# Optimization experiments

Hardware: AMD Instinct MI355X
Metric: run time of the kernel (lower is better)

The kernel has to match this reference:

```python
import jax, jax.numpy as jnp
import numpy as np

N = 50000          # nodes (len(sample.x))
E = 1600000        # edges, avg degree 32
F_IN = 64          # sample.num_node_features
CH = 32            # 4 * 4 * channels_optuna(2)
K = 30000          # ceil(0.6 * N), TopKPooling keep count
FINAL_NODES = 2


def _gelu(v):
    return jax.nn.gelu(v, approximate=False)  # torch F.gelu uses exact erf


def _w(key, shape):
    return jax.random.normal(key, shape, jnp.float32) / np.sqrt(shape[0]).astype(np.float32)


def setup_inputs() -> dict:
    key = jax.random.key(0)
    ks = jax.random.split(key, 16)
    return {
        "x": jax.random.normal(ks[0], (N, F_IN), jnp.float32),
        "edge_index": jax.random.randint(ks[1], (2, E), 0, N, dtype=jnp.int32),
        "wd_root": _w(ks[2], (F_IN, 4)),
        "wd_b": jnp.zeros((4,), jnp.float32),
        "w0_rel": _w(ks[3], (4, CH)),
        "w0_root": _w(ks[4], (4, CH)),
        "w0_b": jnp.zeros((CH,), jnp.float32),
        "w1_rel": _w(ks[5], (CH, 2 * CH)),
        "w1_root": _w(ks[6], (CH, 2 * CH)),
        "w1_b": jnp.zeros((2 * CH,), jnp.float32),
        "w2_rel": _w(ks[7], (2 * CH, 4 * CH)),
        "w2_root": _w(ks[8], (2 * CH, 4 * CH)),
        "w2_b": jnp.zeros((4 * CH,), jnp.float32),
        "pool_p": jax.random.normal(ks[9], (4 * CH,), jnp.float32),
        "w3_rel": _w(ks[10], (4 * CH, 8 * CH)),
        "w3_root": _w(ks[11], (4 * CH, 8 * CH)),
        "w3_b": jnp.zeros((8 * CH,), jnp.float32),
        "w_out": _w(ks[12], (FINAL_NODES * 8 * CH, 1)),
        "b_out": jnp.zeros((1,), jnp.float32),
    }


def _graph_conv(x, src, dst, w_rel, w_root, b, n, mask=None):
    # PyG GraphConv: out_i = W_root x_i + W_rel * sum_{j->i} x_j + b
    msg = x[src]
    if mask is not None:
        msg = msg * mask[:, None]
    agg = jax.ops.segment_sum(msg, dst, num_segments=n)
    return agg @ w_rel + x @ w_root + b


def reference(x, edge_index, wd_root, wd_b, w0_rel, w0_root, w0_b,
              w1_rel, w1_root, w1_b, w2_rel, w2_root, w2_b, pool_p,
              w3_rel, w3_root, w3_b, w_out, b_out):
    src, dst = edge_index[0], edge_index[1]
    # dense_input is GraphConv with empty edge set -> only root term + bias
    h = _gelu(x @ wd_root + wd_b)                                   # [N, 4]
    h = _gelu(_graph_conv(h, src, dst, w0_rel, w0_root, w0_b, N))   # [N, 32]
    h = _gelu(_graph_conv(h, src, dst, w1_rel, w1_root, w1_b, N))   # [N, 64]
    h = _gelu(_graph_conv(h, src, dst, w2_rel, w2_root, w2_b, N))   # [N, 128]
    # TopKPooling(ratio=0.6): score = tanh(x.p/||p||), keep top-K, gate kept x
    score = jnp.tanh(h @ pool_p / jnp.linalg.norm(pool_p))          # [N]
    vals, perm = jax.lax.top_k(score, K)
    hk = h[perm] * vals[:, None]                                    # [K, 128]
    # filter_adj: keep edges with both endpoints selected, remap indices
    node_map = jnp.full((N,), -1, jnp.int32).at[perm].set(jnp.arange(K, dtype=jnp.int32))
    s2, d2 = node_map[src], node_map[dst]
    valid = (s2 >= 0) & (d2 >= 0)
    mask = valid.astype(hk.dtype)
    s2 = jnp.where(valid, s2, 0)
    d2 = jnp.where(valid, d2, 0)
    h2 = _gelu(_graph_conv(hk, s2, d2, w3_rel, w3_root, w3_b, K, mask=mask))  # [K, 256]
    # avg_pool_x with cluster = i % final_nodes (single graph batch)
    cluster = jnp.arange(K, dtype=jnp.int32) % FINAL_NODES
    sums = jax.ops.segment_sum(h2, cluster, num_segments=FINAL_NODES)
    counts = jax.ops.segment_sum(jnp.ones((K,), h2.dtype), cluster, num_segments=FINAL_NODES)
    pooled = sums / counts[:, None]                                  # [2, 256]
    return pooled.reshape(-1) @ w_out + b_out                        # [1]
```

## Files before the change

### kernel.cpp

```cpp
#include <hip/hip_runtime.h>
#include <hip/hip_bf16.h>
#include <math.h>

#define NN 50000
#define EE 1600000
#define KK 30000
#define RTILE 1088
#define NTILES 48
#define CHUNK 16384
#define GBLK 98
#define BKT 391
#define CMAX 6144

typedef __attribute__((ext_vector_type(8))) short bf16x8;
typedef __attribute__((ext_vector_type(4))) float f32x4;

__device__ __forceinline__ float gelu_f(float v) {
  return 0.5f * v * (1.0f + erff(v * 0.70710678118654752440f));
}

__device__ __forceinline__ unsigned short f2bf(float x) {
  __hip_bfloat16 h = __float2bfloat16(x);
  return *(unsigned short*)&h;
}

__device__ __forceinline__ float bf2f(unsigned u16) {
  return __uint_as_float(u16 << 16);
}

__global__ __launch_bounds__(1024) void k_scanA(const unsigned* __restrict__ in, unsigned* __restrict__ out,
                                                unsigned* __restrict__ bsum, int n) {
  __shared__ unsigned sh[1024];
  int t = threadIdx.x;
  int i = blockIdx.x * 1024 + t;
  unsigned v = (i < n) ? in[i] : 0u;
  sh[t] = v;
  __syncthreads();
  for (int ofs = 1; ofs < 1024; ofs <<= 1) {
    unsigned add = (t >= ofs) ? sh[t - ofs] : 0u;
    __syncthreads();
    sh[t] += add;
    __syncthreads();
  }
  if (i < n) out[i] = sh[t] - v;
  if (t == 1023) bsum[blockIdx.x] = sh[1023];
}

__global__ __launch_bounds__(1024) void k_scanB(unsigned* __restrict__ bsum, int nb) {
  __shared__ unsigned sh[1024];
  int t = threadIdx.x;
  unsigned v = (t < nb) ? bsum[t] : 0u;
  sh[t] = v;
  __syncthreads();
  for (int ofs = 1; ofs < 1024; ofs <<= 1) {
    unsigned add = (t >= ofs) ? sh[t - ofs] : 0u;
    __syncthreads();
    sh[t] += add;
    __syncthreads();
  }
  if (t < nb) bsum[t] = sh[t] - v;
}

__global__ __launch_bounds__(1024) void k_scanC(unsigned* __restrict__ out, const unsigned* __restrict__ bsum, int n) {
  int i = blockIdx.x * 1024 + threadIdx.x;
  if (i < n) out[i] += bsum[blockIdx.x];
}

__global__ __launch_bounds__(512) void k_binA(const int* __restrict__ src, const int* __restrict__ dst,
                                              unsigned* __restrict__ chunkEdges, int* __restrict__ chunkBase) {
  __shared__ int hist[BKT];
  __shared__ int scanb[512];
  __shared__ unsigned buf[CHUNK];
  int t = threadIdx.x, g = blockIdx.x;
  int e0 = g * CHUNK;
  int n = EE - e0; if (n > CHUNK) n = CHUNK;
  for (int i = t; i < BKT; i += 512) hist[i] = 0;
  __syncthreads();
  for (int i = t; i < n; i += 512) atomicAdd(&hist[dst[e0 + i] >> 7], 1);
  __syncthreads();
  int v = (t < BKT) ? hist[t] : 0;
  scanb[t] = v;
  __syncthreads();
  for (int ofs = 1; ofs < 512; ofs <<= 1) {
    int a = (t >= ofs) ? scanb[t - ofs] : 0;
    __syncthreads();
    scanb[t] += a;
    __syncthreads();
  }
  if (t < BKT) {
    scanb[t] -= v;
    chunkBase[g * (BKT + 1) + t] = scanb[t];
    hist[t] = 0;
  }
  if (t == 0) chunkBase[g * (BKT + 1) + BKT] = n;
  __syncthreads();
  for (int i = t; i < n; i += 512) {
    int d = dst[e0 + i], s = src[e0 + i];
    int b = d >> 7;
    int pos = scanb[b] + atomicAdd(&hist[b], 1);
    buf[pos] = ((unsigned)(d & 127) << 16) | (unsigned)s;
  }
  __syncthreads();
  for (int i = t; i < n; i += 512) chunkEdges[e0 + i] = buf[i];
}

__global__ __launch_bounds__(512) void k_bktsum(const int* __restrict__ chunkBase, unsigned* __restrict__ bktBase) {
  __shared__ unsigned sh[512];
  int t = threadIdx.x;
  unsigned s = 0;
  if (t < BKT) {
    for (int g = 0; g < GBLK; g++)
      s += (unsigned)(chunkBase[g * (BKT + 1) + t + 1] - chunkBase[g * (BKT + 1) + t]);
  }
  sh[t] = s;
  __syncthreads();
  for (int ofs = 1; ofs < 512; ofs <<= 1) {
    unsigned a = (t >= ofs) ? sh[t - ofs] : 0u;
    __syncthreads();
    sh[t] += a;
    __syncthreads();
  }
  if (t < BKT) bktBase[t] = sh[t] - s;
  if (t == 0) bktBase[BKT] = EE;
}

__global__ __launch_bounds__(256) void k_binC(const unsigned* __restrict__ chunkEdges, const int* __restrict__ chunkBase,
                                              const unsigned* __restrict__ bktBase,
                                              int* __restrict__ rowp, int* __restrict__ csr) {
  __shared__ int segS[GBLK + 1];
  __shared__ int cnt[128];
  __shared__ int loc[128];
  __shared__ unsigned eBuf[CMAX];
  __shared__ int csrB[CMAX];
  int t = threadIdx.x, b = blockIdx.x;
  int n0 = b << 7;
  int nb = NN - n0; if (nb > 128) nb = 128;
  if (t < GBLK) segS[t] = chunkBase[t * (BKT + 1) + b + 1] - chunkBase[t * (BKT + 1) + b];
  if (t < 128) cnt[t] = 0;
  __syncthreads();
  if (t == 0) {
    int run = 0;
    for (int g = 0; g < GBLK; g++) { int L = segS[g]; segS[g] = run; run += L; }
    segS[GBLK] = run;
  }
  __syncthreads();
  int total = segS[GBLK];
  for (int i = t; i < total; i += 256) {
    int lo = 0, hi = GBLK - 1;
    while (lo < hi) { int mid = (lo + hi + 1) >> 1; if (segS[mid] <= i) lo = mid; else hi = mid - 1; }
    int off = chunkBase[lo * (BKT + 1) + b] + (i - segS[lo]);
    unsigned v = chunkEdges[lo * CHUNK + off];
    if (i < CMAX) eBuf[i] = v;
    atomicAdd(&cnt[v >> 16], 1);
  }
  __syncthreads();
  if (t < 128) loc[t] = cnt[t];
  __syncthreads();
  for (int ofs = 1; ofs < 128; ofs <<= 1) {
    int a = (t < 128 && t >= ofs) ? loc[t - ofs] : 0;
    __syncthreads();
    if (t < 128) loc[t] += a;
    __syncthreads();
  }
  if (t < 128) loc[t] -= cnt[t];
  __syncthreads();
  int base = (int)bktBase[b];
  if (t < nb) rowp[n0 + t] = base + loc[t];
  if (b == BKT - 1 && t == 0) rowp[NN] = base + total;
  if (t < 128) cnt[t] = 0;
  __syncthreads();
  for (int i = t; i < total && i < CMAX; i += 256) {
    unsigned v = eBuf[i];
    int d = (int)(v >> 16);
    int pos = loc[d] + atomicAdd(&cnt[d], 1);
    if (pos < CMAX) csrB[pos] = (int)(v & 0xFFFFu);
  }
  __syncthreads();
  for (int i = t; i < total && i < CMAX; i += 256) csr[base + i] = csrB[i];
}

__global__ __launch_bounds__(256) void k_dense(const float* __restrict__ x, const float* __restrict__ w,
                                               const float* __restrict__ b, float* __restrict__ h0) {
  __shared__ float ws[260];
  int t = threadIdx.x;
  ws[t] = w[t];
  if (t < 4) ws[256 + t] = b[t];
  __syncthreads();
  int n = blockIdx.x * 256 + t;
  if (n >= NN) return;
  float acc0 = ws[256], acc1 = ws[257], acc2 = ws[258], acc3 = ws[259];
  const float4* xr = (const float4*)(x + (size_t)n * 64);
#pragma unroll
  for (int k4 = 0; k4 < 16; k4++) {
    float4 v = xr[k4];
    const float* wk = &ws[k4 * 16];
    acc0 += v.x * wk[0];  acc1 += v.x * wk[1];  acc2 += v.x * wk[2];  acc3 += v.x * wk[3];
    acc0 += v.y * wk[4];  acc1 += v.y * wk[5];  acc2 += v.y * wk[6];  acc3 += v.y * wk[7];
    acc0 += v.z * wk[8];  acc1 += v.z * wk[9];  acc2 += v.z * wk[10]; acc3 += v.z * wk[11];
    acc0 += v.w * wk[12]; acc1 += v.w * wk[13]; acc2 += v.w * wk[14]; acc3 += v.w * wk[15];
  }
  float4 o;
  o.x = gelu_f(acc0); o.y = gelu_f(acc1); o.z = gelu_f(acc2); o.w = gelu_f(acc3);
  ((float4*)h0)[n] = o;
}

template <int TPN>
__global__ __launch_bounds__(256) void k_agg(const float* __restrict__ h, const int* __restrict__ rowp,
                                             const int* __restrict__ csr, float* __restrict__ agg) {
  long gt = (long)blockIdx.x * 256 + threadIdx.x;
  int n = (int)(gt / TPN), lane = (int)(gt % TPN);
  if (n >= NN) return;
  int beg = rowp[n], end = rowp[n + 1];
  const float4* hv = (const float4*)h;
  float4 a0 = make_float4(0.f, 0.f, 0.f, 0.f), a1 = a0, a2 = a0, a3 = a0;
  int e = beg;
  for (; e + 4 <= end; e += 4) {
    int s0 = csr[e], s1 = csr[e + 1], s2 = csr[e + 2], s3 = csr[e + 3];
    float4 v0 = hv[(size_t)s0 * TPN + lane];
    float4 v1 = hv[(size_t)s1 * TPN + lane];
    float4 v2 = hv[(size_t)s2 * TPN + lane];
    float4 v3 = hv[(size_t)s3 * TPN + lane];
    a0.x += v0.x; a0.y += v0.y; a0.z += v0.z; a0.w += v0.w;
    a1.x += v1.x; a1.y += v1.y; a1.z += v1.z; a1.w += v1.w;
    a2.x += v2.x; a2.y += v2.y; a2.z += v2.z; a2.w += v2.w;
    a3.x += v3.x; a3.y += v3.y; a3.z += v3.z; a3.w += v3.w;
  }
  for (; e < end; e++) {
    int s = csr[e];
    float4 v = hv[(size_t)s * TPN + lane];
    a0.x += v.x; a0.y += v.y; a0.z += v.z; a0.w += v.w;
  }
  float4 acc;
  acc.x = (a0.x + a1.x) + (a2.x + a3.x);
  acc.y = (a0.y + a1.y) + (a2.y + a3.y);
  acc.z = (a0.z + a1.z) + (a2.z + a3.z);
  acc.w = (a0.w + a1.w) + (a2.w + a3.w);
  ((float4*)agg)[(size_t)n * TPN + lane] = acc;
}

__global__ __launch_bounds__(256) void k_gemm0(const float* __restrict__ agg0, const float* __restrict__ h0,
                                               const float* __restrict__ wrel, const float* __restrict__ wroot,
                                               const float* __restrict__ bias, float* __restrict__ h1) {
  __shared__ float ws[288];
  int t = threadIdx.x;
  if (t < 128) { ws[t] = wrel[t]; ws[128 + t] = wroot[t]; }
  if (t < 32) ws[256 + t] = bias[t];
  __syncthreads();
  int gt = blockIdx.x * 256 + t;
  int n = gt >> 5, j = gt & 31;
  if (n >= NN) return;
  float4 a = ((const float4*)agg0)[n];
  float4 h = ((const float4*)h0)[n];
  float acc = ws[256 + j];
  acc += a.x * ws[j]        + a.y * ws[32 + j]  + a.z * ws[64 + j]  + a.w * ws[96 + j];
  acc += h.x * ws[128 + j]  + h.y * ws[160 + j] + h.z * ws[192 + j] + h.w * ws[224 + j];
  h1[(size_t)n * 32 + j] = gelu_f(acc);
}

template <int DIN, int DOUT>
__global__ __launch_bounds__(256) void k_gemm(const float* __restrict__ Ag, const float* __restrict__ Hp,
                                              const float* __restrict__ Wrel, const float* __restrict__ Wroot,
                                              const float* __restrict__ bias, float* __restrict__ Cout, int R) {
  constexpr int JQ = DOUT / 64;
  __shared__ float As[32][64];
  __shared__ float Ws[32][DOUT];
  int t = threadIdx.x;
  int tx = t & 15, ty = t >> 4;
  int n0 = blockIdx.x * 64;
  int an = t & 63, ac = t >> 6;
  int rowA = n0 + an;
  float acc[JQ][4][4] = {};
  for (int kc = 0; kc < 2 * DIN; kc += 32) {
#pragma unroll
    for (int i = 0; i < 8; i++) {
      int k = ac + 4 * i;
      int kk = kc + k;
      float av = 0.f;
      if (rowA < R) {
        av = (kk < DIN) ? Ag[(size_t)rowA * DIN + kk]
                        : Hp[(size_t)rowA * DIN + (kk - DIN)];
      }
      As[k][an] = av;
    }
    {
      const float* Wsrc = (kc < DIN) ? (Wrel + (size_t)kc * DOUT)
                                     : (Wroot + (size_t)(kc - DIN) * DOUT);
#pragma unroll
      for (int i = 0; i < DOUT / 32; i++) {
        int lin = i * 256 + t;
        int k = lin / (DOUT / 4);
        int col = (lin % (DOUT / 4)) * 4;
        float4 wv = *(const float4*)&Wsrc[(size_t)k * DOUT + col];
        *(float4*)&Ws[k][col] = wv;
      }
    }
    __syncthreads();
#pragma unroll
    for (int k = 0; k < 32; k++) {
      float4 a = *(const float4*)&As[k][4 * ty];
#pragma unroll
      for (int jq = 0; jq < JQ; jq++) {
        float4 w = *(const float4*)&Ws[k][jq * 64 + 4 * tx];
        acc[jq][0][0] += a.x * w.x; acc[jq][0][1] += a.x * w.y; acc[jq][0][2] += a.x * w.z; acc[jq][0][3] += a.x * w.w;
        acc[jq][1][0] += a.y * w.x; acc[jq][1][1] += a.y * w.y; acc[jq][1][2] += a.y * w.z; acc[jq][1][3] += a.y * w.w;
        acc[jq][2][0] += a.z * w.x; acc[jq][2][1] += a.z * w.y; acc[jq][2][2] += a.z * w.z; acc[jq][2][3] += a.z * w.w;
        acc[jq][3][0] += a.w * w.x; acc[jq][3][1] += a.w * w.y; acc[jq][3][2] += a.w * w.z; acc[jq][3][3] += a.w * w.w;
      }
    }
    __syncthreads();
  }
#pragma unroll
  for (int jq = 0; jq < JQ; jq++) {
    int j = jq * 64 + 4 * tx;
#pragma unroll
    for (int r = 0; r < 4; r++) {
      int row = n0 + 4 * ty + r;
      if (row < R) {
        float4 o;
        o.x = gelu_f(acc[jq][r][0] + bias[j]);
        o.y = gelu_f(acc[jq][r][1] + bias[j + 1]);
        o.z = gelu_f(acc[jq][r][2] + bias[j + 2]);
        o.w = gelu_f(acc[jq][r][3] + bias[j + 3]);
        *(float4*)&Cout[(size_t)row * DOUT + j] = o;
      }
    }
  }
}

__global__ __launch_bounds__(256) void k_score(const float* __restrict__ h3, const float* __restrict__ p,
                                               float* __restrict__ score, unsigned* __restrict__ skey,
                                               unsigned* __restrict__ hist) {
  __shared__ float red[256];
  int t = threadIdx.x;
  float pv = 0.f;
  if (t < 128) { float q = p[t]; pv = q * q; }
  red[t] = pv;
  __syncthreads();
  for (int s = 128; s > 0; s >>= 1) { if (t < s) red[t] += red[t + s]; __syncthreads(); }
  float pinv = rsqrtf(red[0]);
  int n = blockIdx.x * 8 + (t >> 5);
  int lane = t & 31;
  if (n >= NN) return;
  float4 hv = ((const float4*)(h3 + (size_t)n * 128))[lane];
  float4 pw = ((const float4*)p)[lane];
  float d = hv.x * pw.x + hv.y * pw.y + hv.z * pw.z + hv.w * pw.w;
  for (int o = 16; o > 0; o >>= 1) d += __shfl_xor(d, o, 32);
  if (lane == 0) {
    float sc = tanhf(d * pinv);
    score[n] = sc;
    unsigned bits = __float_as_uint(sc);
    unsigned mono = (bits & 0x80000000u) ? ~bits : (bits | 0x80000000u);
    unsigned sk = ~mono;
    skey[n] = sk;
    atomicAdd(&hist[(size_t)(n / RTILE) * 65536 + (sk & 0xFFFFu)], 1u);
  }
}

template <int SHIFT>
__global__ __launch_bounds__(256) void k_rhist(const unsigned* __restrict__ keyIn, unsigned* __restrict__ histMat) {
  int gid = blockIdx.x * 256 + threadIdx.x;
  if (gid < NN) {
    unsigned d = (keyIn[gid] >> SHIFT) & 0xFFFFu;
    int tile = gid / RTILE;
    atomicAdd(&histMat[(size_t)tile * 65536 + d], 1u);
  }
}

__global__ __launch_bounds__(256) void k_rtileprefix(unsigned* __restrict__ histMat, unsigned* __restrict__ total) {
  int d = blockIdx.x * 256 + threadIdx.x;
  unsigned run = 0;
  for (int tl = 0; tl < NTILES; tl++) {
    size_t ix = (size_t)tl * 65536 + d;
    unsigned v = histMat[ix];
    histMat[ix] = run;
    run += v;
  }
  total[d] = run;
}

template <int SHIFT, bool FIRST>
__global__ __launch_bounds__(64) void k_rscatter(const unsigned* __restrict__ keyIn, const unsigned* __restrict__ idIn,
                                                 unsigned* __restrict__ histMat, const unsigned* __restrict__ base,
                                                 unsigned* __restrict__ keyOut, unsigned* __restrict__ idOut) {
  int t = threadIdx.x;
  int tile = blockIdx.x;
  for (int c = 0; c < RTILE / 64; c++) {
    int idx = tile * RTILE + c * 64 + t;
    int valid = idx < NN;
    unsigned key = 0u, id = 0u;
    if (valid) {
      key = keyIn[idx];
      id = FIRST ? (unsigned)idx : idIn[idx];
    }
    unsigned d = (key >> SHIFT) & 0xFFFFu;
    unsigned long long same = __ballot(valid != 0);
    if (!valid) same = ~same;
#pragma unroll
    for (int b = 0; b < 16; b++) {
      unsigned long long bb = __ballot((int)((d >> b) & 1u));
      same &= ((d >> b) & 1u) ? bb : ~bb;
    }
    unsigned long long lower = (t == 0) ? 0ull : (same << (64 - t) >> (64 - t));
    unsigned intrar = (unsigned)__popcll(lower);
    unsigned total = (unsigned)__popcll(same);
    int leader = (int)(__ffsll((long long)same) - 1);
    unsigned old = 0u;
    if (valid && t == leader) old = atomicAdd(&histMat[(size_t)tile * 65536 + d], total);
    unsigned basec = (unsigned)__shfl((int)old, leader, 64);
    if (valid) {
      unsigned pos = base[d] + basec + intrar;
      keyOut[pos] = key;
      idOut[pos] = id;
    }
  }
}

__global__ __launch_bounds__(64) void k_rscatter2(const unsigned* __restrict__ keyIn, const unsigned* __restrict__ idIn,
                                                  unsigned* __restrict__ histMat, const unsigned* __restrict__ base,
                                                  int* __restrict__ rank, int* __restrict__ inv) {
  int t = threadIdx.x;
  int tile = blockIdx.x;
  for (int c = 0; c < RTILE / 64; c++) {
    int idx = tile * RTILE + c * 64 + t;
    int valid = idx < NN;
    unsigned key = 0u, id = 0u;
    if (valid) {
      key = keyIn[idx];
      id = idIn[idx];
    }
    unsigned d = key >> 16;
    unsigned long long same = __ballot(valid != 0);
    if (!valid) same = ~same;
#pragma unroll
    for (int b = 0; b < 16; b++) {
      unsigned long long bb = __ballot((int)((d >> b) & 1u));
      same &= ((d >> b) & 1u) ? bb : ~bb;
    }
    unsigned long long lower = (t == 0) ? 0ull : (same << (64 - t) >> (64 - t));
    unsigned intrar = (unsigned)__popcll(lower);
    unsigned total = (unsigned)__popcll(same);
    int leader = (int)(__ffsll((long long)same) - 1);
    unsigned old = 0u;
    if (valid && t == leader) old = atomicAdd(&histMat[(size_t)tile * 65536 + d], total);
    unsigned basec = (unsigned)__shfl((int)old, leader, 64);
    if (valid) {
      unsigned pos = base[d] + basec + intrar;
      rank[(int)id] = (int)pos;
      if (pos < KK) inv[pos] = (int)id;
    }
  }
}

__global__ __launch_bounds__(256) void k_agg3(const int* __restrict__ rank, const int* __restrict__ rowp,
                                              const int* __restrict__ csr, unsigned short* __restrict__ A16) {
  long gt = (long)blockIdx.x * 256 + threadIdx.x;
  int n = (int)(gt >> 4), lane = (int)(gt & 15);
  if (n >= NN) return;
  int r = rank[n];
  if (r >= KK) return;
  int beg = rowp[n], end = rowp[n + 1];
  float a0 = 0.f, a1 = 0.f, a2 = 0.f, a3 = 0.f, a4 = 0.f, a5 = 0.f, a6 = 0.f, a7 = 0.f;
  int e = beg;
  for (; e + 4 <= end; e += 4) {
    int s0 = csr[e], s1 = csr[e + 1], s2 = csr[e + 2], s3 = csr[e + 3];
    int r0 = rank[s0], r1 = rank[s1], r2 = rank[s2], r3 = rank[s3];
    r0 = min(r0, KK); r1 = min(r1, KK); r2 = min(r2, KK); r3 = min(r3, KK);
    uint4 v0 = *(const uint4*)&A16[(size_t)r0 * 256 + 128 + lane * 8];
    uint4 v1 = *(const uint4*)&A16[(size_t)r1 * 256 + 128 + lane * 8];
    uint4 v2 = *(const uint4*)&A16[(size_t)r2 * 256 + 128 + lane * 8];
    uint4 v3 = *(const uint4*)&A16[(size_t)r3 * 256 + 128 + lane * 8];
    a0 += bf2f(v0.x & 0xFFFFu) + bf2f(v1.x & 0xFFFFu) + bf2f(v2.x & 0xFFFFu) + bf2f(v3.x & 0xFFFFu);
    a1 += bf2f(v0.x >> 16)     + bf2f(v1.x >> 16)     + bf2f(v2.x >> 16)     + bf2f(v3.x >> 16);
    a2 += bf2f(v0.y & 0xFFFFu) + bf2f(v1.y & 0xFFFFu) + bf2f(v2.y & 0xFFFFu) + bf2f(v3.y & 0xFFFFu);
    a3 += bf2f(v0.y >> 16)     + bf2f(v1.y >> 16)     + bf2f(v2.y >> 16)     + bf2f(v3.y >> 16);
    a4 += bf2f(v0.z & 0xFFFFu) + bf2f(v1.z & 0xFFFFu) + bf2f(v2.z & 0xFFFFu) + bf2f(v3.z & 0xFFFFu);
    a5 += bf2f(v0.z >> 16)     + bf2f(v1.z >> 16)     + bf2f(v2.z >> 16)     + bf2f(v3.z >> 16);
    a6 += bf2f(v0.w & 0xFFFFu) + bf2f(v1.w & 0xFFFFu) + bf2f(v2.w & 0xFFFFu) + bf2f(v3.w & 0xFFFFu);
    a7 += bf2f(v0.w >> 16)     + bf2f(v1.w >> 16)     + bf2f(v2.w >> 16)     + bf2f(v3.w >> 16);
  }
  for (; e < end; e++) {
    int s = csr[e];
    int rs = min(rank[s], KK);
    uint4 v = *(const uint4*)&A16[(size_t)rs * 256 + 128 + lane * 8];
    a0 += bf2f(v.x & 0xFFFFu); a1 += bf2f(v.x >> 16);
    a2 += bf2f(v.y & 0xFFFFu); a3 += bf2f(v.y >> 16);
    a4 += bf2f(v.z & 0xFFFFu); a5 += bf2f(v.z >> 16);
    a6 += bf2f(v.w & 0xFFFFu); a7 += bf2f(v.w >> 16);
  }
  uint4 o;
  o.x = (unsigned)f2bf(a0) | ((unsigned)f2bf(a1) << 16);
  o.y = (unsigned)f2bf(a2) | ((unsigned)f2bf(a3) << 16);
  o.z = (unsigned)f2bf(a4) | ((unsigned)f2bf(a5) << 16);
  o.w = (unsigned)f2bf(a6) | ((unsigned)f2bf(a7) << 16);
  *(uint4*)&A16[(size_t)r * 256 + lane * 8] = o;
}

__global__ __launch_bounds__(256) void k_gate(const float* __restrict__ h3, const float* __restrict__ scor,
                                              const int* __restrict__ inv, unsigned short* __restrict__ A16) {
  int gt = blockIdx.x * 256 + threadIdx.x;
  int r = gt >> 4, lane = gt & 15;
  if (r > KK) return;
  if (r == KK) {
    *(uint4*)&A16[(size_t)KK * 256 + 128 + lane * 8] = make_uint4(0u, 0u, 0u, 0u);
    return;
  }
  int nd = inv[r];
  float g = scor[nd];
  const float4* src = (const float4*)&h3[(size_t)nd * 128 + lane * 8];
  float4 v0 = src[0], v1 = src[1];
  uint4 o;
  o.x = (unsigned)f2bf(v0.x * g) | ((unsigned)f2bf(v0.y * g) << 16);
  o.y = (unsigned)f2bf(v0.z * g) | ((unsigned)f2bf(v0.w * g) << 16);
  o.z = (unsigned)f2bf(v1.x * g) | ((unsigned)f2bf(v1.y * g) << 16);
  o.w = (unsigned)f2bf(v1.z * g) | ((unsigned)f2bf(v1.w * g) << 16);
  *(uint4*)&A16[(size_t)r * 256 + 128 + lane * 8] = o;
}

__global__ __launch_bounds__(256) void k_wcvt(const float* __restrict__ w3rel, const float* __restrict__ w3root,
                                              unsigned short* __restrict__ W16) {
  int idx = blockIdx.x * 256 + threadIdx.x;
  int k = idx >> 8, c = idx & 255;
  float v = (k < 128) ? w3rel[(size_t)k * 256 + c] : w3root[(size_t)(k - 128) * 256 + c];
  W16[(size_t)c * 256 + k] = f2bf(v);
}

__global__ __launch_bounds__(256) void k_gemm3m(const unsigned short* __restrict__ A16,
                                                const unsigned short* __restrict__ W16,
                                                const float* __restrict__ bias,
                                                float* __restrict__ psum) {
  __shared__ unsigned short Al[64][40];
  __shared__ unsigned short Bl[256][40];
  __shared__ float red[512];
  int t = threadIdx.x;
  int wv = t >> 6, l = t & 63;
  int n0 = blockIdx.x * 64;
  f32x4 acc[4][4];
#pragma unroll
  for (int m = 0; m < 4; m++)
#pragma unroll
    for (int n = 0; n < 4; n++) acc[m][n] = (f32x4){0.f, 0.f, 0.f, 0.f};
  for (int k0 = 0; k0 < 256; k0 += 32) {
    {
      int row = t >> 2, koff = (t & 3) * 8;
      int gr = n0 + row;
      uint4 v = make_uint4(0u, 0u, 0u, 0u);
      if (gr < KK) v = *(const uint4*)&A16[(size_t)gr * 256 + k0 + koff];
      *(uint4*)&Al[row][koff] = v;
    }
    {
      int c0 = t >> 2, slot = t & 3;
#pragma unroll
      for (int i = 0; i < 4; i++) {
        int col = c0 + 64 * i;
        uint4 v = *(const uint4*)&W16[(size_t)col * 256 + k0 + slot * 8];
        *(uint4*)&Bl[col][slot * 8] = v;
      }
    }
    __syncthreads();
    int kf = (l >> 4) * 8;
    bf16x8 a[4], b[4];
#pragma unroll
    for (int m = 0; m < 4; m++) a[m] = *(const bf16x8*)&Al[16 * m + (l & 15)][kf];
#pragma unroll
    for (int n = 0; n < 4; n++) b[n] = *(const bf16x8*)&Bl[wv * 64 + 16 * n + (l & 15)][kf];
#pragma unroll
    for (int m = 0; m < 4; m++)
#pragma unroll
      for (int n = 0; n < 4; n++)
        acc[m][n] = __builtin_amdgcn_mfma_f32_16x16x32_bf16(a[m], b[n], acc[m][n], 0, 0, 0);
    __syncthreads();
  }
  for (int i = t; i < 512; i += 256) red[i] = 0.f;
  __syncthreads();
  int rbase = (l >> 4) * 4;
#pragma unroll
  for (int n = 0; n < 4; n++) {
    int col = wv * 64 + 16 * n + (l & 15);
    float bs = bias[col];
#pragma unroll
    for (int j = 0; j < 4; j++) {
      float s = 0.f;
#pragma unroll
      for (int m = 0; m < 4; m++) {
        int row = n0 + 16 * m + rbase + j;
        if (row < KK) s += gelu_f(acc[m][n][j] + bs);
      }
      atomicAdd(&red[(j & 1) * 256 + col], s);
    }
  }
  __syncthreads();
  for (int i = t; i < 512; i += 256) atomicAdd(&psum[i], red[i]);
}

__global__ __launch_bounds__(512) void k_final(const float* __restrict__ psum, const float* __restrict__ wout,
                                               const float* __restrict__ bout, float* __restrict__ out) {
  __shared__ float red[512];
  int t = threadIdx.x;
  red[t] = psum[t] * (1.0f / 15000.0f) * wout[t];
  __syncthreads();
  for (int s = 256; s > 0; s >>= 1) { if (t < s) red[t] += red[t + s]; __syncthreads(); }
  if (t == 0) out[0] = red[0] + bout[0];
}

extern "C" void kernel_launch(void* const* d_in, const int* in_sizes, int n_in,
                              void* d_out, int out_size, void* d_ws, size_t ws_size,
                              hipStream_t stream) {
  const float* x      = (const float*)d_in[0];
  const int*   ei     = (const int*)d_in[1];
  const float* wdr    = (const float*)d_in[2];
  const float* wdb    = (const float*)d_in[3];
  const float* w0rel  = (const float*)d_in[4];
  const float* w0root = (const float*)d_in[5];
  const float* w0b    = (const float*)d_in[6];
  const float* w1rel  = (const float*)d_in[7];
  const float* w1root = (const float*)d_in[8];
  const float* w1b    = (const float*)d_in[9];
  const float* w2rel  = (const float*)d_in[10];
  const float* w2root = (const float*)d_in[11];
  const float* w2b    = (const float*)d_in[12];
  const float* poolp  = (const float*)d_in[13];
  const float* w3rel  = (const float*)d_in[14];
  const float* w3root = (const float*)d_in[15];
  const float* w3b    = (const float*)d_in[16];
  const float* wout   = (const float*)d_in[17];
  const float* bout   = (const float*)d_in[18];
  float* out = (float*)d_out;

  char* ws = (char*)d_ws;
  size_t o = 0;
  auto alloc = [&](size_t bytes) { size_t r = o; o += (bytes + 255) & ~(size_t)255; return r; };
  size_t o_psum = alloc(512 * 4);
  size_t zbytes = o;
  size_t o_rowp = alloc((size_t)(NN + 1) * 4);
  size_t o_csr  = alloc((size_t)EE * 4);
  size_t o_h0   = alloc((size_t)NN * 4 * 4);
  size_t o_h1   = alloc((size_t)NN * 32 * 4);
  size_t o_h2   = alloc((size_t)NN * 64 * 4);
  size_t o_h3   = alloc((size_t)NN * 128 * 4);
  size_t o_agg  = alloc((size_t)NN * 64 * 4);
  size_t o_scor = alloc((size_t)NN * 4);
  size_t o_skey = alloc((size_t)NN * 4);
  size_t o_rank = alloc((size_t)NN * 4);
  size_t o_inv  = alloc((size_t)KK * 4);
  size_t o_keyB = alloc((size_t)NN * 4);
  size_t o_idB  = alloc((size_t)NN * 4);
  size_t o_tot  = alloc(65536 * 4);
  size_t o_bsB  = alloc(1024 * 4);
  size_t o_W16  = alloc((size_t)256 * 256 * 2);
  size_t o_cbase = alloc((size_t)GBLK * (BKT + 1) * 4);
  size_t o_bbase = alloc((size_t)(BKT + 1) * 4);
  (void)ws_size; (void)in_sizes; (void)n_in; (void)out_size;

  float*    psum = (float*)(ws + o_psum);
  int*      rowp = (int*)(ws + o_rowp);
  int*      csr  = (int*)(ws + o_csr);
  float*    h0   = (float*)(ws + o_h0);
  float*    h1   = (float*)(ws + o_h1);
  float*    h2   = (float*)(ws + o_h2);
  float*    h3   = (float*)(ws + o_h3);
  float*    agg  = (float*)(ws + o_agg);
  float*    scor = (float*)(ws + o_scor);
  unsigned* skey = (unsigned*)(ws + o_skey);
  int*      rank = (int*)(ws + o_rank);
  int*      inv  = (int*)(ws + o_inv);
  unsigned* keyB = (unsigned*)(ws + o_keyB);
  unsigned* idB  = (unsigned*)(ws + o_idB);
  unsigned* tot  = (unsigned*)(ws + o_tot);
  unsigned* bsB  = (unsigned*)(ws + o_bsB);
  unsigned* hist = (unsigned*)(ws + o_h2);
  unsigned short* A16 = (unsigned short*)(ws + o_h1);
  unsigned short* W16 = (unsigned short*)(ws + o_W16);
  unsigned* chunkEdges = (unsigned*)(ws + o_agg);
  int*      chunkBase  = (int*)(ws + o_cbase);
  unsigned* bktBase    = (unsigned*)(ws + o_bbase);

  hipMemsetAsync(ws, 0, zbytes, stream);

  const int* src = ei;
  const int* dstp = ei + EE;

  k_binA<<<GBLK, 512, 0, stream>>>(src, dstp, chunkEdges, chunkBase);
  k_bktsum<<<1, 512, 0, stream>>>(chunkBase, bktBase);
  k_binC<<<BKT, 256, 0, stream>>>(chunkEdges, chunkBase, bktBase, rowp, csr);

  k_dense<<<(NN + 255) / 256, 256, 0, stream>>>(x, wdr, wdb, h0);

  k_agg<1><<<(NN + 255) / 256, 256, 0, stream>>>(h0, rowp, csr, agg);
  k_gemm0<<<(NN * 32 + 255) / 256, 256, 0, stream>>>(agg, h0, w0rel, w0root, w0b, h1);

  k_agg<8><<<(NN * 8 + 255) / 256, 256, 0, stream>>>(h1, rowp, csr, agg);
  k_gemm<32, 64><<<(NN + 63) / 64, 256, 0, stream>>>(agg, h1, w1rel, w1root, w1b, h2, NN);

  k_agg<16><<<(NN * 16 + 255) / 256, 256, 0, stream>>>(h2, rowp, csr, agg);
  k_gemm<64, 128><<<(NN + 63) / 64, 256, 0, stream>>>(agg, h2, w2rel, w2root, w2b, h3, NN);

  hipMemsetAsync(hist, 0, (size_t)NTILES * 65536 * 4, stream);
  k_score<<<(NN + 7) / 8, 256, 0, stream>>>(h3, poolp, scor, skey, hist);

  k_rtileprefix<<<65536 / 256, 256, 0, stream>>>(hist, tot);
  k_scanA<<<64, 1024, 0, stream>>>(tot, tot, bsB, 65536);
  k_scanB<<<1, 1024, 0, stream>>>(bsB, 64);
  k_scanC<<<64, 1024, 0, stream>>>(tot, bsB, 65536);
  k_rscatter<0, true><<<NTILES, 64, 0, stream>>>(skey, nullptr, hist, tot, keyB, idB);

  hipMemsetAsync(hist, 0, (size_t)NTILES * 65536 * 4, stream);
  k_rhist<16><<<(NN + 255) / 256, 256, 0, stream>>>(keyB, hist);
  k_rtileprefix<<<65536 / 256, 256, 0, stream>>>(hist, tot);
  k_scanA<<<64, 1024, 0, stream>>>(tot, tot, bsB, 65536);
  k_scanB<<<1, 1024, 0, stream>>>(bsB, 64);
  k_scanC<<<64, 1024, 0, stream>>>(tot, bsB, 65536);
  k_rscatter2<<<NTILES, 64, 0, stream>>>(keyB, idB, hist, tot, rank, inv);

  k_wcvt<<<256, 256, 0, stream>>>(w3rel, w3root, W16);
  k_gate<<<((KK + 1) * 16 + 255) / 256, 256, 0, stream>>>(h3, scor, inv, A16);
  k_agg3<<<((long)NN * 16 + 255) / 256, 256, 0, stream>>>(rank, rowp, csr, A16);
  k_gemm3m<<<(KK + 63) / 64, 256, 0, stream>>>(A16, W16, w3b, psum);

  k_final<<<1, 512, 0, stream>>>(psum, wout, bout, out);
}
```

Baseline: 509.5 us.

## Switch layer-1/2 GraphConv GEMMs from FP32 FMA to bf16 MFMA

Replaces the FP32 register-tiled GEMM for the 32->64 and 64->128 GraphConv layers with an MFMA 16x16x32 bf16 kernel. The concatenated rel/root weights are pre-transposed to bf16 in small new kernels, and activations are converted to bf16 while being staged into LDS. The goal is to move the dense matmul work onto the matrix cores and cut the ALU cost. The cost is bf16 rounding error in the layer-1/2 activations, which feed the top-k selection. The w3 weight conversion is also moved earlier in the stream.

```diff
diff --git a/kernel.cpp b/kernel.cpp
--- a/kernel.cpp
+++ b/kernel.cpp
@@ -258,70 +258,79 @@
 }
 
 template <int DIN, int DOUT>
-__global__ __launch_bounds__(256) void k_gemm(const float* __restrict__ Ag, const float* __restrict__ Hp,
-                                              const float* __restrict__ Wrel, const float* __restrict__ Wroot,
-                                              const float* __restrict__ bias, float* __restrict__ Cout, int R) {
-  constexpr int JQ = DOUT / 64;
-  __shared__ float As[32][64];
-  __shared__ float Ws[32][DOUT];
-  int t = threadIdx.x;
-  int tx = t & 15, ty = t >> 4;
+__global__ __launch_bounds__(256) void k_wcvtT(const float* __restrict__ wrel, const float* __restrict__ wroot,
+                                               unsigned short* __restrict__ W16T) {
+  constexpr int K = 2 * DIN;
+  int idx = blockIdx.x * 256 + threadIdx.x;
+  int col = idx / K, k = idx % K;
+  float v = (k < DIN) ? wrel[(size_t)k * DOUT + col] : wroot[(size_t)(k - DIN) * DOUT + col];
+  W16T[(size_t)col * K + k] = f2bf(v);
+}
+
+template <int DIN, int DOUT>
+__global__ __launch_bounds__(256) void k_gemmM(const float* __restrict__ Ag, const float* __restrict__ Hp,
+                                               const unsigned short* __restrict__ W16T,
+                                               const float* __restrict__ bias, float* __restrict__ Cout, int R) {
+  constexpr int K = 2 * DIN;
+  constexpr int NF = DOUT / 64;
+  constexpr int WSTR = K + 8;
+  __shared__ unsigned short Al[64][40];
+  __shared__ unsigned short Wl[DOUT][WSTR];
+  int t = threadIdx.x;
+  int wv = t >> 6, l = t & 63;
   int n0 = blockIdx.x * 64;
-  int an = t & 63, ac = t >> 6;
-  int rowA = n0 + an;
-  float acc[JQ][4][4] = {};
-  for (int kc = 0; kc < 2 * DIN; kc += 32) {
-#pragma unroll
-    for (int i = 0; i < 8; i++) {
-      int k = ac + 4 * i;
-      int kk = kc + k;
-      float av = 0.f;
-      if (rowA < R) {
-        av = (kk < DIN) ? Ag[(size_t)rowA * DIN + kk]
-                        : Hp[(size_t)rowA * DIN + (kk - DIN)];
-      }
-      As[k][an] = av;
-    }
-    {
-      const float* Wsrc = (kc < DIN) ? (Wrel + (size_t)kc * DOUT)
-                                     : (Wroot + (size_t)(kc - DIN) * DOUT);
-#pragma unroll
-      for (int i = 0; i < DOUT / 32; i++) {
-        int lin = i * 256 + t;
-        int k = lin / (DOUT / 4);
-        int col = (lin % (DOUT / 4)) * 4;
-        float4 wv = *(const float4*)&Wsrc[(size_t)k * DOUT + col];
-        *(float4*)&Ws[k][col] = wv;
-      }
-    }
-    __syncthreads();
-#pragma unroll
-    for (int k = 0; k < 32; k++) {
-      float4 a = *(const float4*)&As[k][4 * ty];
-#pragma unroll
-      for (int jq = 0; jq < JQ; jq++) {
-        float4 w = *(const float4*)&Ws[k][jq * 64 + 4 * tx];
-        acc[jq][0][0] += a.x * w.x; acc[jq][0][1] += a.x * w.y; acc[jq][0][2] += a.x * w.z; acc[jq][0][3] += a.x * w.w;
-        acc[jq][1][0] += a.y * w.x; acc[jq][1][1] += a.y * w.y; acc[jq][1][2] += a.y * w.z; acc[jq][1][3] += a.y * w.w;
-        acc[jq][2][0] += a.z * w.x; acc[jq][2][1] += a.z * w.y; acc[jq][2][2] += a.z * w.z; acc[jq][2][3] += a.z * w.w;
-        acc[jq][3][0] += a.w * w.x; acc[jq][3][1] += a.w * w.y; acc[jq][3][2] += a.w * w.z; acc[jq][3][3] += a.w * w.w;
-      }
-    }
-    __syncthreads();
-  }
-#pragma unroll
-  for (int jq = 0; jq < JQ; jq++) {
-    int j = jq * 64 + 4 * tx;
-#pragma unroll
-    for (int r = 0; r < 4; r++) {
-      int row = n0 + 4 * ty + r;
-      if (row < R) {
-        float4 o;
-        o.x = gelu_f(acc[jq][r][0] + bias[j]);
-        o.y = gelu_f(acc[jq][r][1] + bias[j + 1]);
-        o.z = gelu_f(acc[jq][r][2] + bias[j + 2]);
-        o.w = gelu_f(acc[jq][r][3] + bias[j + 3]);
-        *(float4*)&Cout[(size_t)row * DOUT + j] = o;
+  for (int i = t; i < DOUT * (K / 8); i += 256) {
+    int col = i / (K / 8), ks = i % (K / 8);
+    uint4 v = *(const uint4*)&W16T[(size_t)col * K + ks * 8];
+    *(uint4*)&Wl[col][ks * 8] = v;
+  }
+  f32x4 acc[4][NF];
+#pragma unroll
+  for (int m = 0; m < 4; m++)
+#pragma unroll
+    for (int n = 0; n < NF; n++) acc[m][n] = (f32x4){0.f, 0.f, 0.f, 0.f};
+  int row = t >> 2, koff = (t & 3) * 8;
+  int gr = n0 + row;
+  for (int kc = 0; kc < K; kc += 32) {
+    const float* srcp = (kc < DIN) ? Ag : Hp;
+    int kbase = (kc < DIN) ? kc : (kc - DIN);
+    float4 v0 = make_float4(0.f, 0.f, 0.f, 0.f), v1 = v0;
+    if (gr < R) {
+      const float* rp = srcp + (size_t)gr * DIN + kbase + koff;
+      v0 = *(const float4*)rp;
+      v1 = *(const float4*)(rp + 4);
+    }
+    uint4 p;
+    p.x = (unsigned)f2bf(v0.x) | ((unsigned)f2bf(v0.y) << 16);
+    p.y = (unsigned)f2bf(v0.z) | ((unsigned)f2bf(v0.w) << 16);
+    p.z = (unsigned)f2bf(v1.x) | ((unsigned)f2bf(v1.y) << 16);
+    p.w = (unsigned)f2bf(v1.z) | ((unsigned)f2bf(v1.w) << 16);
+    *(uint4*)&Al[row][koff] = p;
+    __syncthreads();
+    int kf = (l >> 4) * 8;
+    bf16x8 a[4], b[NF];
+#pragma unroll
+    for (int m = 0; m < 4; m++) a[m] = *(const bf16x8*)&Al[16 * m + (l & 15)][kf];
+#pragma unroll
+    for (int n = 0; n < NF; n++) b[n] = *(const bf16x8*)&Wl[wv * (DOUT / 4) + 16 * n + (l & 15)][kc + kf];
+#pragma unroll
+    for (int m = 0; m < 4; m++)
+#pragma unroll
+      for (int n = 0; n < NF; n++)
+        acc[m][n] = __builtin_amdgcn_mfma_f32_16x16x32_bf16(a[m], b[n], acc[m][n], 0, 0, 0);
+    __syncthreads();
+  }
+  int rb = (l >> 4) * 4;
+#pragma unroll
+  for (int n = 0; n < NF; n++) {
+    int col = wv * (DOUT / 4) + 16 * n + (l & 15);
+    float bs = bias[col];
+#pragma unroll
+    for (int m = 0; m < 4; m++) {
+#pragma unroll
+      for (int j = 0; j < 4; j++) {
+        int r = n0 + 16 * m + rb + j;
+        if (r < R) Cout[(size_t)r * DOUT + col] = gelu_f(acc[m][n][j] + bs);
       }
     }
   }
@@ -647,6 +656,8 @@
   size_t o_tot  = alloc(65536 * 4);
   size_t o_bsB  = alloc(1024 * 4);
   size_t o_W16  = alloc((size_t)256 * 256 * 2);
+  size_t o_W1T  = alloc((size_t)64 * 64 * 2);
+  size_t o_W2T  = alloc((size_t)128 * 128 * 2);
   size_t o_cbase = alloc((size_t)GBLK * (BKT + 1) * 4);
   size_t o_bbase = alloc((size_t)(BKT + 1) * 4);
   (void)ws_size; (void)in_sizes; (void)n_in; (void)out_size;
@@ -670,6 +681,8 @@
   unsigned* hist = (unsigned*)(ws + o_h2);
   unsigned short* A16 = (unsigned short*)(ws + o_h1);
   unsigned short* W16 = (unsigned short*)(ws + o_W16);
+  unsigned short* W1T = (unsigned short*)(ws + o_W1T);
+  unsigned short* W2T = (unsigned short*)(ws + o_W2T);
   unsigned* chunkEdges = (unsigned*)(ws + o_agg);
   int*      chunkBase  = (int*)(ws + o_cbase);
   unsigned* bktBase    = (unsigned*)(ws + o_bbase);
@@ -683,16 +696,20 @@
   k_bktsum<<<1, 512, 0, stream>>>(chunkBase, bktBase);
   k_binC<<<BKT, 256, 0, stream>>>(chunkEdges, chunkBase, bktBase, rowp, csr);
 
+  k_wcvtT<32, 64><<<(64 * 64) / 256, 256, 0, stream>>>(w1rel, w1root, W1T);
+  k_wcvtT<64, 128><<<(128 * 128) / 256, 256, 0, stream>>>(w2rel, w2root, W2T);
+  k_wcvt<<<256, 256, 0, stream>>>(w3rel, w3root, W16);
+
   k_dense<<<(NN + 255) / 256, 256, 0, stream>>>(x, wdr, wdb, h0);
 
   k_agg<1><<<(NN + 255) / 256, 256, 0, stream>>>(h0, rowp, csr, agg);
   k_gemm0<<<(NN * 32 + 255) / 256, 256, 0, stream>>>(agg, h0, w0rel, w0root, w0b, h1);
 
   k_agg<8><<<(NN * 8 + 255) / 256, 256, 0, stream>>>(h1, rowp, csr, agg);
-  k_gemm<32, 64><<<(NN + 63) / 64, 256, 0, stream>>>(agg, h1, w1rel, w1root, w1b, h2, NN);
+  k_gemmM<32, 64><<<(NN + 63) / 64, 256, 0, stream>>>(agg, h1, W1T, w1b, h2, NN);
 
   k_agg<16><<<(NN * 16 + 255) / 256, 256, 0, stream>>>(h2, rowp, csr, agg);
-  k_gemm<64, 128><<<(NN + 63) / 64, 256, 0, stream>>>(agg, h2, w2rel, w2root, w2b, h3, NN);
+  k_gemmM<64, 128><<<(NN + 63) / 64, 256, 0, stream>>>(agg, h2, W2T, w2b, h3, NN);
 
   hipMemsetAsync(hist, 0, (size_t)NTILES * 65536 * 4, stream);
   k_score<<<(NN + 7) / 8, 256, 0, stream>>>(h3, poolp, scor, skey, hist);
@@ -711,7 +728,6 @@
   k_scanC<<<64, 1024, 0, stream>>>(tot, bsB, 65536);
   k_rscatter2<<<NTILES, 64, 0, stream>>>(keyB, idB, hist, tot, rank, inv);
 
-  k_wcvt<<<256, 256, 0, stream>>>(w3rel, w3root, W16);
   k_gate<<<((KK + 1) * 16 + 255) / 256, 256, 0, stream>>>(h3, scor, inv, A16);
   k_agg3<<<((long)NN * 16 + 255) / 256, 256, 0, stream>>>(rank, rowp, csr, A16);
   k_gemm3m<<<(KK + 63) / 64, 256, 0, stream>>>(A16, W16, w3b, psum);
```

Result: no change. 515.0 us (+1.1%).
